# Performance work log

Hardware: AMD Instinct MI355X
Metric: run time of the kernel (lower is better)

The kernel has to match this reference:

```python
import jax, jax.numpy as jnp
import numpy as np

N, E, G = 25000, 50000, 1000   # nodes, edges, graphs
NP, EP = 25, 50                # nodes/edges per graph
D = 64                         # node_out_feats


def setup_inputs() -> dict:
    key = jax.random.key(0)
    ks = jax.random.split(key, 32)
    rng = np.random.RandomState(0)
    # edges stay within their graph (molecular batch structure)
    base = np.repeat(np.arange(G), EP) * NP
    src = jnp.asarray(base + rng.randint(0, NP, E), dtype=jnp.int32)
    dst = jnp.asarray(base + rng.randint(0, NP, E), dtype=jnp.int32)
    graph_ids = jnp.repeat(jnp.arange(G, dtype=jnp.int32), NP)

    def p(i, shape, s=0.05):
        return (jax.random.normal(ks[i], shape, jnp.float32) * s)

    return dict(
        n_feats=jax.random.normal(ks[0], (N, 74), jnp.float32),
        e_feats=jax.random.normal(ks[1], (E, 12), jnp.float32),
        src=src, dst=dst, graph_ids=graph_ids,
        # project_node_feats: Linear(74,64)+ReLU
        proj_W=p(2, (74, D)), proj_b=jnp.zeros((D,), jnp.float32),
        # NNConv edge network: Linear(12,64)+ReLU+Linear(64,64*64)
        eW1=p(3, (12, D)), eb1=jnp.zeros((D,), jnp.float32),
        eW2=p(4, (D, D * D)), eb2=jnp.zeros((D * D,), jnp.float32),
        conv_b=jnp.zeros((D,), jnp.float32),
        # GRU (1 layer, gates r,z,n) stored transposed: x @ W
        gru_Wi=p(5, (D, 3 * D)), gru_Wh=p(6, (D, 3 * D)),
        gru_bi=jnp.zeros((3 * D,), jnp.float32), gru_bh=jnp.zeros((3 * D,), jnp.float32),
        # Set2Set LSTM: 3 layers, input 2D (layer0) / D, hidden D, gates i,f,g,o
        lWi0=p(7, (2 * D, 4 * D)), lWh0=p(8, (D, 4 * D)), lb0=jnp.zeros((4 * D,), jnp.float32),
        lWi1=p(9, (D, 4 * D)), lWh1=p(10, (D, 4 * D)), lb1=jnp.zeros((4 * D,), jnp.float32),
        lWi2=p(11, (D, 4 * D)), lWh2=p(12, (D, 4 * D)), lb2=jnp.zeros((4 * D,), jnp.float32),
        # predict hidden: Linear(128,64)+ReLU, then head fc: Linear(64,1)
        pW=p(13, (2 * D, D)), pb=jnp.zeros((D,), jnp.float32),
        fW=p(14, (D, 1)), fb=jnp.zeros((1,), jnp.float32),
    )


def reference(n_feats, e_feats, src, dst, graph_ids,
              proj_W, proj_b, eW1, eb1, eW2, eb2, conv_b,
              gru_Wi, gru_Wh, gru_bi, gru_bh,
              lWi0, lWh0, lb0, lWi1, lWh1, lb1, lWi2, lWh2, lb2,
              pW, pb, fW, fb):
    # --- MPNNGNN ---
    h = jax.nn.relu(n_feats @ proj_W + proj_b)                      # (N, D)
    W_e = (jax.nn.relu(e_feats @ eW1 + eb1) @ eW2 + eb2).reshape(E, D, D)
    g = h                                                            # GRU hidden init = node feats
    for _ in range(3):
        msg = jnp.einsum('ei,eio->eo', h[src], W_e)                  # per-edge message
        m = jax.nn.relu(jax.ops.segment_sum(msg, dst, num_segments=N) + conv_b)
        gi = m @ gru_Wi + gru_bi
        gh = g @ gru_Wh + gru_bh
        ir, iz, inn = jnp.split(gi, 3, -1)
        hr, hz, hn = jnp.split(gh, 3, -1)
        r = jax.nn.sigmoid(ir + hr)
        z = jax.nn.sigmoid(iz + hz)
        nn_ = jnp.tanh(inn + r * hn)
        g = (1.0 - z) * nn_ + z * g
        h = g
    # --- Set2Set readout (3 iters, 3-layer LSTM) ---
    Wis, Whs, bs = [lWi0, lWi1, lWi2], [lWh0, lWh1, lWh2], [lb0, lb1, lb2]
    hs = [jnp.zeros((G, D), h.dtype) for _ in range(3)]
    cs = [jnp.zeros((G, D), h.dtype) for _ in range(3)]
    q_star = jnp.zeros((G, 2 * D), h.dtype)
    for _ in range(3):
        x = q_star
        for l in range(3):
            gates = x @ Wis[l] + hs[l] @ Whs[l] + bs[l]
            i, f, gg, o = jnp.split(gates, 4, -1)
            cs[l] = jax.nn.sigmoid(f) * cs[l] + jax.nn.sigmoid(i) * jnp.tanh(gg)
            hs[l] = jax.nn.sigmoid(o) * jnp.tanh(cs[l])
            x = hs[l]
        q = x                                                        # (G, D)
        e = jnp.sum(h * q[graph_ids], -1)                            # (N,)
        e = e - jax.ops.segment_max(e, graph_ids, num_segments=G)[graph_ids]
        ex = jnp.exp(e)
        alpha = ex / jax.ops.segment_sum(ex, graph_ids, num_segments=G)[graph_ids]
        rdt = jax.ops.segment_sum(alpha[:, None] * h, graph_ids, num_segments=G)
        q_star = jnp.concatenate([q, rdt], -1)                       # (G, 2D)
    # --- predict hidden + head ---
    graph_feats = jax.nn.relu(q_star @ pW + pb)                      # (G, D)
    return jax.nn.sigmoid(graph_feats @ fW + fb)[:, 0]               # (G,)
```

## Files before the change

### kernel.cpp

```cpp
#include <hip/hip_runtime.h>
#include <math.h>

__device__ __forceinline__ float sigf(float x) { return 1.f / (1.f + expf(-x)); }

using half8v = __attribute__((ext_vector_type(8))) _Float16;
using f32x4  = __attribute__((ext_vector_type(4))) float;
using f32x16 = __attribute__((ext_vector_type(16))) float;

__device__ __forceinline__ unsigned short f2h(float x) {
    union { _Float16 h; unsigned short u; } c; c.h = (_Float16)x; return c.u;
}

template<int K, int MODE>
__global__ __launch_bounds__(256, 4)
void rowmat_relu_t(const float* __restrict__ in, const float* __restrict__ W,
                   const float* __restrict__ b, float* __restrict__ out32,
                   _Float16* __restrict__ out16, int R)
{
    __shared__ float Wl[K * 64];
    __shared__ float rowsS[32 * K];

    const int tid  = threadIdx.x;
    const int row0 = blockIdx.x * 32;

    for (int i = tid; i < K * 64; i += 256)
        Wl[i] = W[i];
    const int lim = (R - row0 >= 32 ? 32 : (R - row0)) * K;
    for (int i = tid; i < 32 * K; i += 256)
        rowsS[i] = (i < lim) ? in[(size_t)row0 * K + i] : 0.f;
    __syncthreads();

    const int wave = tid >> 6, lane = tid & 63;
    const float bv = b[lane];

    float acc[8];
    #pragma unroll
    for (int rr = 0; rr < 8; ++rr) acc[rr] = bv;

    #pragma unroll 2
    for (int k = 0; k < K; ++k) {
        const float wv = Wl[k * 64 + lane];
        #pragma unroll
        for (int rr = 0; rr < 8; ++rr)
            acc[rr] = fmaf(rowsS[(wave * 8 + rr) * K + k], wv, acc[rr]);
    }

    #pragma unroll
    for (int rr = 0; rr < 8; ++rr) {
        const int row = row0 + wave * 8 + rr;
        if (row < R) {
            const float v = fmaxf(acc[rr], 0.f);
            if (MODE == 0) out32[(size_t)row * 64 + lane] = v;
            out16[(size_t)row * 64 + lane] = (_Float16)v;
        }
    }
}

__global__ __launch_bounds__(256)
void prep_w_kernel(const float* __restrict__ eW2, const float* __restrict__ eb2,
                   unsigned short* __restrict__ w_staged)
{
    int slot = blockIdx.x * 256 + threadIdx.x;
    if (slot >= 65 * 512) return;
    int kc  = slot >> 9;
    int s   = slot & 511;
    int o   = s >> 3, seg = s & 7;
    unsigned int packed[4];
    #pragma unroll
    for (int p = 0; p < 4; ++p) {
        int j0 = kc * 64 + seg * 8 + p * 2;
        float v0 = (j0     < 4096) ? eW2[(size_t)j0 * 64 + o]       : eb2[(size_t)(j0 - 4096) * 64 + o];
        float v1 = (j0 + 1 < 4096) ? eW2[(size_t)(j0 + 1) * 64 + o] : eb2[(size_t)(j0 + 1 - 4096) * 64 + o];
        packed[p] = (unsigned int)f2h(v0) | ((unsigned int)f2h(v1) << 16);
    }
    int dstb = ((o * 128) + seg * 16) ^ ((o & 7) << 4);
    uint4 st = {packed[0], packed[1], packed[2], packed[3]};
    *(uint4*)((char*)w_staged + (size_t)kc * 8192 + dstb) = st;
}

__global__ __launch_bounds__(256)
void prep_gruw_kernel(const float* __restrict__ Wi, const float* __restrict__ Wh,
                      _Float16* __restrict__ WiT, _Float16* __restrict__ WhT)
{
    int idx = blockIdx.x * 256 + threadIdx.x;
    if (idx >= 2 * 12288) return;
    const float* W = (idx < 12288) ? Wi : Wh;
    _Float16*    O = (idx < 12288) ? WiT : WhT;
    int r = idx & 12287;
    int n = r >> 6, k = r & 63;
    O[n * 64 + k] = (_Float16)W[(size_t)k * 192 + n];
}

__global__ __launch_bounds__(256)
void prep_s2sw_kernel(const float* __restrict__ lWi0, const float* __restrict__ lWh0,
                      const float* __restrict__ lWi1, const float* __restrict__ lWh1,
                      const float* __restrict__ lWi2, const float* __restrict__ lWh2,
                      _Float16* __restrict__ WB0, _Float16* __restrict__ WB1,
                      _Float16* __restrict__ WB2)
{
    int idx = blockIdx.x * 256 + threadIdx.x;
    if (idx < 49152) {
        int k = idx >> 8, n = idx & 255;
        float v = (k < 128) ? lWi0[(size_t)k * 256 + n] : lWh0[(size_t)(k - 128) * 256 + n];
        WB0[((k >> 3) * 2048) + n * 8 + (k & 7)] = (_Float16)v;
    } else if (idx < 81920) {
        int r = idx - 49152;
        int k = r >> 8, n = r & 255;
        float v = (k < 64) ? lWi1[(size_t)k * 256 + n] : lWh1[(size_t)(k - 64) * 256 + n];
        WB1[((k >> 3) * 2048) + n * 8 + (k & 7)] = (_Float16)v;
    } else if (idx < 114688) {
        int r = idx - 81920;
        int k = r >> 8, n = r & 255;
        float v = (k < 64) ? lWi2[(size_t)k * 256 + n] : lWh2[(size_t)(k - 64) * 256 + n];
        WB2[((k >> 3) * 2048) + n * 8 + (k & 7)] = (_Float16)v;
    }
}

__global__ __launch_bounds__(256, 3)
void msg_mfma_kernel(const _Float16* __restrict__ t16, const _Float16* __restrict__ h16,
                     const int* __restrict__ src, const int* __restrict__ dst,
                     const unsigned short* __restrict__ w_staged,
                     float* __restrict__ msum, int E)
{
    __shared__ _Float16 tS[64 * 70];
    __shared__ __align__(16) unsigned short bbuf[3][4096];

    const int tid  = threadIdx.x;
    const int lane = tid & 63;
    const int wave = tid >> 6;
    const int wm   = wave & 1, wn = wave >> 1;
    const int e0   = blockIdx.x * 64;

    #pragma unroll
    for (int p = 0; p < 2; ++p) {
        int slot = tid + p * 256;
        int e = slot >> 3, k0 = (slot & 7) * 8;
        int ee = e0 + e;
        half8v tv8 = (half8v)(_Float16)0.f;
        if (ee < E) tv8 = ((const half8v*)(t16 + (size_t)ee * 64))[slot & 7];
        #pragma unroll
        for (int j = 0; j < 8; ++j)
            tS[(k0 + j) * 70 + e] = tv8[j];
    }

    const int erow = wm * 32 + (lane & 31);
    const int ee   = e0 + erow;
    const int sidx = (ee < E) ? src[ee] : 0;
    const half8v* hp = (const half8v*)(h16 + (size_t)sidx * 64);
    half8v Hh[4];
    #pragma unroll
    for (int s = 0; s < 4; ++s)
        Hh[s] = hp[s * 2 + (lane >> 5)];

    const uint4* wsrc = (const uint4*)w_staged;
    {
        uint4 c00 = wsrc[tid], c01 = wsrc[256 + tid];
        ((uint4*)bbuf[0])[tid]       = c00;
        ((uint4*)bbuf[0])[256 + tid] = c01;
    }
    uint4 pA0 = wsrc[512 + tid],  pA1 = wsrc[512 + 256 + tid];
    uint4 pB0 = wsrc[1024 + tid], pB1 = wsrc[1024 + 256 + tid];

    f32x16 acc;
    #pragma unroll
    for (int r = 0; r < 16; ++r) acc[r] = 0.f;

    const int colg  = wn * 32 + (lane & 31);
    const int bbase = (colg * 128) ^ ((colg & 7) << 4);

    __syncthreads();

    int cur = 0;
    for (int kc = 0; kc < 65; ++kc) {
        const _Float16 tv = (kc < 64) ? tS[kc * 70 + erow] : (_Float16)1.0f;
        const char* bb = (const char*)bbuf[cur];
        #pragma unroll
        for (int s = 0; s < 4; ++s) {
            half8v af = Hh[s] * tv;
            half8v bf = *(const half8v*)(bb + (bbase + s * 32 + (lane >> 5) * 16));
            acc = __builtin_amdgcn_mfma_f32_32x32x16_f16(af, bf, acc, 0, 0, 0);
        }
        const int nxt = (cur == 2) ? 0 : cur + 1;
        if (kc < 64) {
            ((uint4*)bbuf[nxt])[tid]       = pA0;
            ((uint4*)bbuf[nxt])[256 + tid] = pA1;
            pA0 = pB0; pA1 = pB1;
            if (kc + 3 <= 64) {
                pB0 = wsrc[(size_t)(kc + 3) * 512 + tid];
                pB1 = wsrc[(size_t)(kc + 3) * 512 + 256 + tid];
            }
        }
        __syncthreads();
        cur = nxt;
    }

    #pragma unroll
    for (int r = 0; r < 16; ++r) {
        const int row  = (r & 3) + 8 * (r >> 2) + 4 * (lane >> 5);
        const int edge = e0 + wm * 32 + row;
        if (edge < E)
            atomicAdd(&msum[(size_t)dst[edge] * 64 + colg], acc[r]);
    }
}

__global__ __launch_bounds__(256, 2)
void gru_mfma_kernel(const float* __restrict__ msum, float* __restrict__ h,
                     _Float16* __restrict__ h16,
                     const _Float16* __restrict__ WiT, const _Float16* __restrict__ WhT,
                     const float* __restrict__ bi, const float* __restrict__ bh,
                     const float* __restrict__ conv_b, int N)
{
    __shared__ _Float16 BtI[192 * 72];
    __shared__ _Float16 BtH[192 * 72];
    __shared__ _Float16 Am[64 * 72];
    __shared__ _Float16 Ah[64 * 72];

    const int tid  = threadIdx.x;
    const int lane = tid & 63;
    const int wave = tid >> 6;
    const int m0   = wave * 16;
    const int row0 = blockIdx.x * 64;

    #pragma unroll
    for (int p = 0; p < 6; ++p) {
        int slot = tid + p * 256;
        int n = slot >> 3, k0 = (slot & 7) * 8;
        uint4 vi = ((const uint4*)WiT)[slot];
        uint4 vh = ((const uint4*)WhT)[slot];
        *(uint4*)&BtI[n * 72 + k0] = vi;
        *(uint4*)&BtH[n * 72 + k0] = vh;
    }
    #pragma unroll
    for (int p = 0; p < 4; ++p) {
        int idx = tid + p * 256;
        int r = idx >> 4, k4 = (idx & 15) * 4;
        int row = row0 + r;
        float4 mv = make_float4(0.f, 0.f, 0.f, 0.f);
        if (row < N) mv = *(const float4*)&msum[(size_t)row * 64 + k4];
        float4 cb = *(const float4*)&conv_b[k4];
        union { _Float16 hx[4]; uint2 u2; } pk;
        pk.hx[0] = (_Float16)fmaxf(mv.x + cb.x, 0.f);
        pk.hx[1] = (_Float16)fmaxf(mv.y + cb.y, 0.f);
        pk.hx[2] = (_Float16)fmaxf(mv.z + cb.z, 0.f);
        pk.hx[3] = (_Float16)fmaxf(mv.w + cb.w, 0.f);
        *(uint2*)&Am[r * 72 + k4] = pk.u2;
    }
    #pragma unroll
    for (int p = 0; p < 2; ++p) {
        int idx = tid + p * 256;
        int r = idx >> 3, k0 = (idx & 7) * 8;
        int row = row0 + r;
        uint4 v = {0u, 0u, 0u, 0u};
        if (row < N) v = *(const uint4*)&h16[(size_t)row * 64 + k0];
        *(uint4*)&Ah[r * 72 + k0] = v;
    }
    __syncthreads();

    const int l15 = lane & 15;

    f32x4 acc_i[12], acc_h[12];
    #pragma unroll
    for (int nt = 0; nt < 12; ++nt) {
        #pragma unroll
        for (int j = 0; j < 4; ++j) { acc_i[nt][j] = 0.f; acc_h[nt][j] = 0.f; }
    }

    #pragma unroll
    for (int ks = 0; ks < 2; ++ks) {
        const int ka = ks * 32 + (lane >> 4) * 8;
        half8v am = *(const half8v*)&Am[(m0 + l15) * 72 + ka];
        half8v ah = *(const half8v*)&Ah[(m0 + l15) * 72 + ka];
        #pragma unroll
        for (int nt = 0; nt < 12; ++nt) {
            half8v b_i = *(const half8v*)&BtI[(nt * 16 + l15) * 72 + ka];
            half8v b_h = *(const half8v*)&BtH[(nt * 16 + l15) * 72 + ka];
            acc_i[nt] = __builtin_amdgcn_mfma_f32_16x16x32_f16(am, b_i, acc_i[nt], 0, 0, 0);
            acc_h[nt] = __builtin_amdgcn_mfma_f32_16x16x32_f16(ah, b_h, acc_h[nt], 0, 0, 0);
        }
    }

    const int rgrp = lane >> 4;
    #pragma unroll
    for (int nt0 = 0; nt0 < 4; ++nt0) {
        const int c = nt0 * 16 + l15;
        const float bir = bi[c],        bhr = bh[c];
        const float biz = bi[64 + c],   bhz = bh[64 + c];
        const float bin = bi[128 + c],  bhn = bh[128 + c];
        #pragma unroll
        for (int j = 0; j < 4; ++j) {
            const int row = row0 + m0 + rgrp * 4 + j;
            if (row >= N) continue;
            float rg = sigf(acc_i[nt0][j]      + bir + acc_h[nt0][j]      + bhr);
            float zg = sigf(acc_i[4 + nt0][j]  + biz + acc_h[4 + nt0][j]  + bhz);
            float ng = tanhf(acc_i[8 + nt0][j] + bin + rg * (acc_h[8 + nt0][j] + bhn));
            float hold = h[(size_t)row * 64 + c];
            float hv = (1.f - zg) * ng + zg * hold;
            h[(size_t)row * 64 + c]   = hv;
            h16[(size_t)row * 64 + c] = (_Float16)hv;
        }
    }
}

__device__ __forceinline__ float gate_dot8(const _Float16* __restrict__ WB,
                                           int tid, const float* __restrict__ xs,
                                           int nblk)
{
    float a0 = 0.f, a1 = 0.f, a2 = 0.f, a3 = 0.f;
    #pragma unroll 4
    for (int b = 0; b < nblk; ++b) {
        half8v w = *(const half8v*)(WB + (size_t)b * 2048 + tid * 8);
        float4 xa = *(const float4*)&xs[b * 8];
        float4 xb = *(const float4*)&xs[b * 8 + 4];
        a0 = fmaf((float)w[0], xa.x, a0);
        a1 = fmaf((float)w[1], xa.y, a1);
        a2 = fmaf((float)w[2], xa.z, a2);
        a3 = fmaf((float)w[3], xa.w, a3);
        a0 = fmaf((float)w[4], xb.x, a0);
        a1 = fmaf((float)w[5], xb.y, a1);
        a2 = fmaf((float)w[6], xb.z, a2);
        a3 = fmaf((float)w[7], xb.w, a3);
    }
    return (a0 + a1) + (a2 + a3);
}

__global__ __launch_bounds__(256)
void set2set_kernel(const float* __restrict__ h,
                    const _Float16* __restrict__ WB0, const _Float16* __restrict__ WB1,
                    const _Float16* __restrict__ WB2,
                    const float* __restrict__ lb0, const float* __restrict__ lb1,
                    const float* __restrict__ lb2,
                    const float* __restrict__ pW, const float* __restrict__ pb,
                    const float* __restrict__ fW, const float* __restrict__ fb,
                    float* __restrict__ out)
{
    const int g   = blockIdx.x;
    const int tid = threadIdx.x;

    __shared__ float hl[25 * 65];
    __shared__ float hs[3][64], cs[3][64];
    __shared__ float qstar[128];
    __shared__ __align__(16) float xs[192];
    __shared__ float gates[256];
    __shared__ float als[32];

    for (int idx = tid; idx < 25 * 64; idx += 256) {
        int n = idx >> 6, d = idx & 63;
        hl[n * 65 + d] = h[((size_t)g * 25 + n) * 64 + d];
    }
    if (tid < 128) qstar[tid] = 0.f;
    if (tid < 64) {
        #pragma unroll
        for (int l = 0; l < 3; ++l) { hs[l][tid] = 0.f; cs[l][tid] = 0.f; }
    }
    __syncthreads();

    for (int it = 0; it < 3; ++it) {
        if (tid < 128) xs[tid] = qstar[tid];
        else if (tid < 192) xs[tid] = hs[0][tid - 128];
        __syncthreads();
        gates[tid] = lb0[tid] + gate_dot8(WB0, tid, xs, 24);
        __syncthreads();
        if (tid < 64) {
            float ig = sigf(gates[tid]);
            float fg = sigf(gates[64 + tid]);
            float gg = tanhf(gates[128 + tid]);
            float og = sigf(gates[192 + tid]);
            float cv = fg * cs[0][tid] + ig * gg;
            cs[0][tid] = cv;
            hs[0][tid] = og * tanhf(cv);
        }
        __syncthreads();
        if (tid < 64) xs[tid] = hs[0][tid];
        else if (tid < 128) xs[tid] = hs[1][tid - 64];
        __syncthreads();
        gates[tid] = lb1[tid] + gate_dot8(WB1, tid, xs, 16);
        __syncthreads();
        if (tid < 64) {
            float ig = sigf(gates[tid]);
            float fg = sigf(gates[64 + tid]);
            float gg = tanhf(gates[128 + tid]);
            float og = sigf(gates[192 + tid]);
            float cv = fg * cs[1][tid] + ig * gg;
            cs[1][tid] = cv;
            hs[1][tid] = og * tanhf(cv);
        }
        __syncthreads();
        if (tid < 64) xs[tid] = hs[1][tid];
        else if (tid < 128) xs[tid] = hs[2][tid - 64];
        __syncthreads();
        gates[tid] = lb2[tid] + gate_dot8(WB2, tid, xs, 16);
        __syncthreads();
        if (tid < 64) {
            float ig = sigf(gates[tid]);
            float fg = sigf(gates[64 + tid]);
            float gg = tanhf(gates[128 + tid]);
            float og = sigf(gates[192 + tid]);
            float cv = fg * cs[2][tid] + ig * gg;
            cs[2][tid] = cv;
            hs[2][tid] = og * tanhf(cv);
        }
        __syncthreads();
        float ev = -1e30f;
        if (tid < 25) {
            float acc = 0.f;
            for (int d = 0; d < 64; ++d)
                acc = fmaf(hl[tid * 65 + d], hs[2][d], acc);
            ev = acc;
        }
        if (tid < 64) {
            float mx = ev;
            #pragma unroll
            for (int off = 16; off; off >>= 1) mx = fmaxf(mx, __shfl_xor(mx, off, 32));
            float ex = (tid < 25) ? expf(ev - mx) : 0.f;
            float sm = ex;
            #pragma unroll
            for (int off = 16; off; off >>= 1) sm += __shfl_xor(sm, off, 32);
            if (tid < 25) als[tid] = ex / sm;
        }
        __syncthreads();
        if (tid < 64) {
            float rdt = 0.f;
            #pragma unroll
            for (int n = 0; n < 25; ++n) rdt = fmaf(als[n], hl[n * 65 + tid], rdt);
            qstar[tid]      = hs[2][tid];
            qstar[64 + tid] = rdt;
        }
        __syncthreads();
    }

    if (tid < 64) {
        float acc = pb[tid];
        #pragma unroll 8
        for (int k = 0; k < 128; ++k)
            acc = fmaf(qstar[k], pW[(size_t)k * 64 + tid], acc);
        float part = fmaxf(acc, 0.f) * fW[tid];
        #pragma unroll
        for (int off = 32; off; off >>= 1) part += __shfl_xor(part, off, 64);
        if (tid == 0) out[g] = 1.f / (1.f + expf(-(part + fb[0])));
    }
}

extern "C" void kernel_launch(void* const* d_in, const int* in_sizes, int n_in,
                              void* d_out, int out_size, void* d_ws, size_t ws_size,
                              hipStream_t stream)
{
    const float* n_feats = (const float*)d_in[0];
    const float* e_feats = (const float*)d_in[1];
    const int*   src     = (const int*)d_in[2];
    const int*   dst     = (const int*)d_in[3];
    const float* proj_W  = (const float*)d_in[5];
    const float* proj_b  = (const float*)d_in[6];
    const float* eW1     = (const float*)d_in[7];
    const float* eb1     = (const float*)d_in[8];
    const float* eW2     = (const float*)d_in[9];
    const float* eb2     = (const float*)d_in[10];
    const float* conv_b  = (const float*)d_in[11];
    const float* gWi     = (const float*)d_in[12];
    const float* gWh     = (const float*)d_in[13];
    const float* gbi     = (const float*)d_in[14];
    const float* gbh     = (const float*)d_in[15];
    const float* lWi0    = (const float*)d_in[16];
    const float* lWh0    = (const float*)d_in[17];
    const float* lb0     = (const float*)d_in[18];
    const float* lWi1    = (const float*)d_in[19];
    const float* lWh1    = (const float*)d_in[20];
    const float* lb1     = (const float*)d_in[21];
    const float* lWi2    = (const float*)d_in[22];
    const float* lWh2    = (const float*)d_in[23];
    const float* lb2     = (const float*)d_in[24];
    const float* pW      = (const float*)d_in[25];
    const float* pb      = (const float*)d_in[26];
    const float* fW      = (const float*)d_in[27];
    const float* fb      = (const float*)d_in[28];

    const int N = in_sizes[0] / 74;
    const int E = in_sizes[1] / 12;
    const int G = out_size;

    float* ws   = (float*)d_ws;
    float* h    = ws;
    float* msum = h + (size_t)N * 64;
    _Float16* h16 = (_Float16*)(msum + (size_t)N * 64);
    _Float16* t16 = h16 + (size_t)N * 64;
    unsigned short* w_staged = (unsigned short*)(t16 + (size_t)E * 64);
    _Float16* WiT = (_Float16*)(w_staged + 65 * 4096);
    _Float16* WhT = WiT + 12288;
    _Float16* WB0 = WhT + 12288;
    _Float16* WB1 = WB0 + 49152;
    _Float16* WB2 = WB1 + 32768;

    prep_w_kernel<<<130, 256, 0, stream>>>(eW2, eb2, w_staged);
    prep_gruw_kernel<<<96, 256, 0, stream>>>(gWi, gWh, WiT, WhT);
    prep_s2sw_kernel<<<448, 256, 0, stream>>>(lWi0, lWh0, lWi1, lWh1, lWi2, lWh2,
                                              WB0, WB1, WB2);

    rowmat_relu_t<74, 0><<<(N + 31) / 32, 256, 0, stream>>>(n_feats, proj_W, proj_b, h, h16, N);
    rowmat_relu_t<12, 1><<<(E + 31) / 32, 256, 0, stream>>>(e_feats, eW1, eb1, nullptr, t16, E);

    for (int it = 0; it < 3; ++it) {
        hipMemsetAsync(msum, 0, (size_t)N * 64 * sizeof(float), stream);
        msg_mfma_kernel<<<(E + 63) / 64, 256, 0, stream>>>(t16, h16, src, dst, w_staged, msum, E);
        gru_mfma_kernel<<<(N + 63) / 64, 256, 0, stream>>>(msum, h, h16, WiT, WhT,
                                                           gbi, gbh, conv_b, N);
    }

    set2set_kernel<<<G, 256, 0, stream>>>(h, WB0, WB1, WB2, lb0, lb1, lb2,
                                          pW, pb, fW, fb, (float*)d_out);
}
```

Before: 285.0 us.

## Stream edge-network weights directly from global into MFMA registers, dropping LDS staging

The message kernel no longer copies the per-chunk fp16 weight tiles into a triple-buffered LDS ring with a block barrier every chunk. Instead, each wave loads its B fragments straight from global memory in a register-level 4-deep prefetch, using 16x16x32 MFMA tiles. The prep kernel is changed so the staged weights are laid out in exactly the per-lane order those loads expect. This removes LDS traffic and the 65 barriers, but it increases register pressure, and each block now reads its weights from L2/global.

```diff
diff --git a/kernel.cpp b/kernel.cpp
--- a/kernel.cpp
+++ b/kernel.cpp
@@ -5,10 +5,12 @@
 
 using half8v = __attribute__((ext_vector_type(8))) _Float16;
 using f32x4  = __attribute__((ext_vector_type(4))) float;
-using f32x16 = __attribute__((ext_vector_type(16))) float;
 
 __device__ __forceinline__ unsigned short f2h(float x) {
     union { _Float16 h; unsigned short u; } c; c.h = (_Float16)x; return c.u;
+}
+__device__ __forceinline__ half8v u2h(uint4 v) {
+    union { uint4 u; half8v h; } c; c.u = v; return c.h;
 }
 
 template<int K, int MODE>
@@ -62,20 +64,24 @@
 {
     int slot = blockIdx.x * 256 + threadIdx.x;
     if (slot >= 65 * 512) return;
-    int kc  = slot >> 9;
-    int s   = slot & 511;
-    int o   = s >> 3, seg = s & 7;
+    int kc   = slot >> 9;
+    int s    = slot & 511;
+    int sub  = s >> 6, lane = s & 63;
+    int wn   = sub >> 2, tn = (sub >> 1) & 1, ks = sub & 1;
+    int kg   = lane >> 4, l15 = lane & 15;
+    int o    = wn * 32 + tn * 16 + l15;
+    int seg  = kg + ks * 4;
+    int j0   = kc * 64 + seg * 8;
     unsigned int packed[4];
     #pragma unroll
     for (int p = 0; p < 4; ++p) {
-        int j0 = kc * 64 + seg * 8 + p * 2;
-        float v0 = (j0     < 4096) ? eW2[(size_t)j0 * 64 + o]       : eb2[(size_t)(j0 - 4096) * 64 + o];
-        float v1 = (j0 + 1 < 4096) ? eW2[(size_t)(j0 + 1) * 64 + o] : eb2[(size_t)(j0 + 1 - 4096) * 64 + o];
+        int j = j0 + p * 2;
+        float v0 = (j     < 4096) ? eW2[(size_t)j * 64 + o]       : eb2[(size_t)(j - 4096) * 64 + o];
+        float v1 = (j + 1 < 4096) ? eW2[(size_t)(j + 1) * 64 + o] : eb2[(size_t)(j + 1 - 4096) * 64 + o];
         packed[p] = (unsigned int)f2h(v0) | ((unsigned int)f2h(v1) << 16);
     }
-    int dstb = ((o * 128) + seg * 16) ^ ((o & 7) << 4);
     uint4 st = {packed[0], packed[1], packed[2], packed[3]};
-    *(uint4*)((char*)w_staged + (size_t)kc * 8192 + dstb) = st;
+    ((uint4*)w_staged)[slot] = st;
 }
 
 __global__ __launch_bounds__(256)
@@ -123,7 +129,6 @@
                      float* __restrict__ msum, int E)
 {
     __shared__ _Float16 tS[64 * 70];
-    __shared__ __align__(16) unsigned short bbuf[3][4096];
 
     const int tid  = threadIdx.x;
     const int lane = tid & 63;
@@ -143,63 +148,89 @@
             tS[(k0 + j) * 70 + e] = tv8[j];
     }
 
-    const int erow = wm * 32 + (lane & 31);
-    const int ee   = e0 + erow;
-    const int sidx = (ee < E) ? src[ee] : 0;
-    const half8v* hp = (const half8v*)(h16 + (size_t)sidx * 64);
-    half8v Hh[4];
-    #pragma unroll
-    for (int s = 0; s < 4; ++s)
-        Hh[s] = hp[s * 2 + (lane >> 5)];
-
-    const uint4* wsrc = (const uint4*)w_staged;
+    const int l15 = lane & 15;
+    const int kg  = lane >> 4;
+
+    half8v Hh[2][2];
+    #pragma unroll
+    for (int tm = 0; tm < 2; ++tm) {
+        const int edge = e0 + wm * 32 + tm * 16 + l15;
+        const int sidx = (edge < E) ? src[edge] : 0;
+        const half8v* hp = (const half8v*)(h16 + (size_t)sidx * 64);
+        Hh[tm][0] = hp[kg];
+        Hh[tm][1] = hp[kg + 4];
+    }
+
+    const uint4* W4  = (const uint4*)w_staged;
+    const int    wb  = wn * 256 + lane;
+
+    uint4 S0a, S0b, S0c, S0d, S1a, S1b, S1c, S1d;
+    uint4 S2a, S2b, S2c, S2d, S3a, S3b, S3c, S3d;
+
+#define LOADC(A, B, C, D, cc)                                         \
+    { size_t off = (size_t)(cc) * 512 + wb;                           \
+      A = W4[off]; B = W4[off + 64]; C = W4[off + 128]; D = W4[off + 192]; }
+
+#define COMP(A, B, C, D, TV0, TV1)                                            \
+    { half8v af00 = Hh[0][0] * (TV0), af01 = Hh[0][1] * (TV0);                \
+      half8v af10 = Hh[1][0] * (TV1), af11 = Hh[1][1] * (TV1);                \
+      half8v b00 = u2h(A), b01 = u2h(B), b10 = u2h(C), b11 = u2h(D);          \
+      acc00 = __builtin_amdgcn_mfma_f32_16x16x32_f16(af00, b00, acc00, 0,0,0);\
+      acc01 = __builtin_amdgcn_mfma_f32_16x16x32_f16(af00, b10, acc01, 0,0,0);\
+      acc10 = __builtin_amdgcn_mfma_f32_16x16x32_f16(af10, b00, acc10, 0,0,0);\
+      acc11 = __builtin_amdgcn_mfma_f32_16x16x32_f16(af10, b10, acc11, 0,0,0);\
+      acc00 = __builtin_amdgcn_mfma_f32_16x16x32_f16(af01, b01, acc00, 0,0,0);\
+      acc01 = __builtin_amdgcn_mfma_f32_16x16x32_f16(af01, b11, acc01, 0,0,0);\
+      acc10 = __builtin_amdgcn_mfma_f32_16x16x32_f16(af11, b01, acc10, 0,0,0);\
+      acc11 = __builtin_amdgcn_mfma_f32_16x16x32_f16(af11, b11, acc11, 0,0,0); }
+
+    LOADC(S0a, S0b, S0c, S0d, 0)
+    LOADC(S1a, S1b, S1c, S1d, 1)
+    LOADC(S2a, S2b, S2c, S2d, 2)
+    LOADC(S3a, S3b, S3c, S3d, 3)
+
+    f32x4 acc00, acc01, acc10, acc11;
+    #pragma unroll
+    for (int j = 0; j < 4; ++j) { acc00[j] = 0.f; acc01[j] = 0.f; acc10[j] = 0.f; acc11[j] = 0.f; }
+
+    __syncthreads();
+
+    const int tvb0 = wm * 32 + l15, tvb1 = wm * 32 + 16 + l15;
+
+    for (int c = 0; c < 64; c += 4) {
+        _Float16 ta0 = tS[(c + 0) * 70 + tvb0], tb0 = tS[(c + 0) * 70 + tvb1];
+        _Float16 ta1 = tS[(c + 1) * 70 + tvb0], tb1 = tS[(c + 1) * 70 + tvb1];
+        _Float16 ta2 = tS[(c + 2) * 70 + tvb0], tb2 = tS[(c + 2) * 70 + tvb1];
+        _Float16 ta3 = tS[(c + 3) * 70 + tvb0], tb3 = tS[(c + 3) * 70 + tvb1];
+
+        COMP(S0a, S0b, S0c, S0d, ta0, tb0)
+        if (c + 4 <= 64) LOADC(S0a, S0b, S0c, S0d, c + 4)
+        COMP(S1a, S1b, S1c, S1d, ta1, tb1)
+        if (c + 5 <= 64) LOADC(S1a, S1b, S1c, S1d, c + 5)
+        COMP(S2a, S2b, S2c, S2d, ta2, tb2)
+        if (c + 6 <= 64) LOADC(S2a, S2b, S2c, S2d, c + 6)
+        COMP(S3a, S3b, S3c, S3d, ta3, tb3)
+        if (c + 7 <= 64) LOADC(S3a, S3b, S3c, S3d, c + 7)
+    }
     {
-        uint4 c00 = wsrc[tid], c01 = wsrc[256 + tid];
-        ((uint4*)bbuf[0])[tid]       = c00;
-        ((uint4*)bbuf[0])[256 + tid] = c01;
-    }
-    uint4 pA0 = wsrc[512 + tid],  pA1 = wsrc[512 + 256 + tid];
-    uint4 pB0 = wsrc[1024 + tid], pB1 = wsrc[1024 + 256 + tid];
-
-    f32x16 acc;
-    #pragma unroll
-    for (int r = 0; r < 16; ++r) acc[r] = 0.f;
-
-    const int colg  = wn * 32 + (lane & 31);
-    const int bbase = (colg * 128) ^ ((colg & 7) << 4);
-
-    __syncthreads();
-
-    int cur = 0;
-    for (int kc = 0; kc < 65; ++kc) {
-        const _Float16 tv = (kc < 64) ? tS[kc * 70 + erow] : (_Float16)1.0f;
-        const char* bb = (const char*)bbuf[cur];
-        #pragma unroll
-        for (int s = 0; s < 4; ++s) {
-            half8v af = Hh[s] * tv;
-            half8v bf = *(const half8v*)(bb + (bbase + s * 32 + (lane >> 5) * 16));
-            acc = __builtin_amdgcn_mfma_f32_32x32x16_f16(af, bf, acc, 0, 0, 0);
-        }
-        const int nxt = (cur == 2) ? 0 : cur + 1;
-        if (kc < 64) {
-            ((uint4*)bbuf[nxt])[tid]       = pA0;
-            ((uint4*)bbuf[nxt])[256 + tid] = pA1;
-            pA0 = pB0; pA1 = pB1;
-            if (kc + 3 <= 64) {
-                pB0 = wsrc[(size_t)(kc + 3) * 512 + tid];
-                pB1 = wsrc[(size_t)(kc + 3) * 512 + 256 + tid];
-            }
-        }
-        __syncthreads();
-        cur = nxt;
-    }
-
-    #pragma unroll
-    for (int r = 0; r < 16; ++r) {
-        const int row  = (r & 3) + 8 * (r >> 2) + 4 * (lane >> 5);
-        const int edge = e0 + wm * 32 + row;
-        if (edge < E)
-            atomicAdd(&msum[(size_t)dst[edge] * 64 + colg], acc[r]);
+        const _Float16 one = (_Float16)1.0f;
+        COMP(S0a, S0b, S0c, S0d, one, one)
+    }
+#undef LOADC
+#undef COMP
+
+    f32x4 acc[2][2] = {{acc00, acc01}, {acc10, acc11}};
+    #pragma unroll
+    for (int tm = 0; tm < 2; ++tm) {
+        #pragma unroll
+        for (int j = 0; j < 4; ++j) {
+            const int edge = e0 + wm * 32 + tm * 16 + kg * 4 + j;
+            if (edge >= E) continue;
+            const int d = dst[edge];
+            #pragma unroll
+            for (int tn = 0; tn < 2; ++tn)
+                atomicAdd(&msum[(size_t)d * 64 + wn * 32 + tn * 16 + l15], acc[tm][tn][j]);
+        }
     }
 }
 
```

Measured after the change: 268.3 us. -5.8%, faster.
